# Optimization experiments

Measured on AMD Instinct MI355X. Metric: run time of the kernel, lower is better.

Reference implementation:

```python
import jax, jax.numpy as jnp
import numpy as np

B, N, C = 8, 100000, 90          # batch, total anchors over all levels, num_classes (COCO)
SCORE_THR = 0.05                  # pre_nms_score_threshold
IOU_THR = 0.5                     # nms_iou_threshold
MAX_DET = 100                     # max_num_detections (per class and total)
PRE_NMS_K = 512                   # per-class candidate cap before greedy NMS
NEG = -1e9                        # suppressed-score sentinel


def setup_inputs() -> dict:
    key = jax.random.key(0)
    kb, ks = jax.random.split(key)
    raw = jax.random.uniform(kb, (B, N, 1, 4), dtype=jnp.float32) * 512.0
    # build valid [y1, x1, y2, x2] boxes from the rand fill
    y1 = jnp.minimum(raw[..., 0], raw[..., 2])
    y2 = jnp.maximum(raw[..., 0], raw[..., 2])
    x1 = jnp.minimum(raw[..., 1], raw[..., 3])
    x2 = jnp.maximum(raw[..., 1], raw[..., 3])
    boxes = jnp.stack([y1, x1, y2, x2], axis=-1)            # [B, N, 1, 4]
    scores = jax.random.uniform(ks, (B, N, C), dtype=jnp.float32)  # [B, N, C]
    return {"boxes": boxes, "scores": scores}


def _iou_one_vs_all(box, boxes):
    # box: [4], boxes: [K, 4], layout (y1, x1, y2, x2)
    yy1 = jnp.maximum(box[0], boxes[:, 0])
    xx1 = jnp.maximum(box[1], boxes[:, 1])
    yy2 = jnp.minimum(box[2], boxes[:, 2])
    xx2 = jnp.minimum(box[3], boxes[:, 3])
    inter = jnp.clip(yy2 - yy1, 0.0) * jnp.clip(xx2 - xx1, 0.0)
    area = (box[2] - box[0]) * (box[3] - box[1])
    areas = (boxes[:, 2] - boxes[:, 0]) * (boxes[:, 3] - boxes[:, 1])
    return inter / (area + areas - inter + 1e-8)


def _nms_single(cboxes, cscores):
    # Greedy per-class NMS: cboxes [K,4], cscores [K] -> MAX_DET boxes/scores.
    K = cboxes.shape[0]
    idxs = jnp.arange(K)

    def step(active, _):
        j = jnp.argmax(active)
        s = active[j]
        b = cboxes[j]
        iou = _iou_one_vs_all(b, cboxes)
        sup = (iou > IOU_THR) | (idxs == j)
        return jnp.where(sup, NEG, active), (b, s)

    _, (sel_boxes, sel_scores) = jax.lax.scan(step, cscores, None, length=MAX_DET)
    return sel_boxes, sel_scores  # [MAX_DET, 4], [MAX_DET]


def _detections(boxes, scores):
    bx = boxes[:, :, 0, :]                                   # class-agnostic boxes [B, N, 4]
    sm = jnp.where(scores >= SCORE_THR, scores, NEG)         # score thresholding
    st = jnp.transpose(sm, (0, 2, 1))                        # [B, C, N]
    cscores, cidx = jax.lax.top_k(st, PRE_NMS_K)             # [B, C, K]
    cboxes = jax.vmap(lambda b, i: b[i])(bx, cidx)           # [B, C, K, 4]
    sel_boxes, sel_scores = jax.vmap(jax.vmap(_nms_single))(cboxes, cscores)
    cls = jnp.broadcast_to(jnp.arange(C)[None, :, None], (B, C, MAX_DET))
    fs = sel_scores.reshape(B, -1)                           # [B, C*MAX_DET]
    fb = sel_boxes.reshape(B, -1, 4)
    fc = cls.reshape(B, -1)
    top_s, top_i = jax.lax.top_k(fs, MAX_DET)                # top MAX_DET over all classes
    top_b = jnp.take_along_axis(fb, top_i[..., None], axis=1)
    top_c = jnp.take_along_axis(fc, top_i, axis=1)
    valid = top_s >= SCORE_THR
    out_boxes = jnp.where(valid[..., None], top_b, 0.0)     # [B, MAX_DET, 4]
    out_scores = jnp.where(valid, top_s, 0.0)               # [B, MAX_DET]
    out_classes = jnp.where(valid, top_c, 0).astype(jnp.int32)
    num_valid = valid.sum(axis=1).astype(jnp.int32)         # [B]
    return out_boxes, out_scores, out_classes, num_valid


def reference(boxes, scores):
    return _detections(boxes, scores)
```

## Files before the change

kernel.cpp:

```cpp
#include <hip/hip_runtime.h>

#define NB 8
#define NN 100000
#define NC 90
#define SCORE_THR 0.05f
#define IOU_THR 0.5f
#define MAX_DET 100
#define PRE_NMS_K 512
#define NEGV -1000000000.0f
#define T0 0.9925f
#define CAP 1024
#define NBC (NB * NC)
#define CNT_STRIDE 16
#define CHUNK 1024
#define NCHUNK 98
#define LCAP 32
#define IOU_CMP_C 0x1.0000008p-1

typedef float f32x4 __attribute__((ext_vector_type(4)));

__device__ __forceinline__ unsigned ordf(float s) {
    unsigned u = __float_as_uint(s);
    return (u & 0x80000000u) ? ~u : (u | 0x80000000u);
}
__device__ __forceinline__ float deordf(unsigned o) {
    return (o & 0x80000000u) ? __uint_as_float(o ^ 0x80000000u) : __uint_as_float(~o);
}
__device__ __forceinline__ unsigned long long mkkey(float s, unsigned idx) {
    return ((unsigned long long)ordf(s) << 32) | (unsigned long long)(0xFFFFFFFFu - idx);
}

__global__ __launch_bounds__(256) void k_zero(uint4* __restrict__ cnt4, uint4* __restrict__ ovf4) {
    unsigned i = blockIdx.x * 256u + threadIdx.x;
    if (i < (NBC * CNT_STRIDE) / 4) cnt4[i] = make_uint4(0u, 0u, 0u, 0u);
    if (i < NBC / 4) ovf4[i] = make_uint4(0u, 0u, 0u, 0u);
}

__global__ __launch_bounds__(512) void k_collect(const float* __restrict__ scores,
                                                 unsigned* __restrict__ cnt,
                                                 unsigned* __restrict__ ovf,
                                                 unsigned long long* __restrict__ buf) {
    __shared__ unsigned long long lst[NC][LCAP + 1];
    __shared__ unsigned lcnt[NC];
    int b = blockIdx.x / NCHUNK;
    int chunk = blockIdx.x - b * NCHUNK;
    int n0 = chunk * CHUNK;
    const f32x4* base4 = reinterpret_cast<const f32x4*>(scores + ((size_t)b * NN + n0) * NC);

    for (int i = threadIdx.x; i < NC; i += 512) lcnt[i] = 0u;
    __syncthreads();

    auto process = [&](f32x4 v, int idx) {
        #pragma unroll
        for (int e = 0; e < 4; ++e) {
            float s = v[e];
            if (s >= T0) {
                int local = 4 * idx + e;
                int c = local % NC;
                int n = n0 + local / NC;
                unsigned slot = atomicAdd(&lcnt[c], 1u);
                if (slot < LCAP) lst[c][slot] = mkkey(s, (unsigned)n);
                else atomicOr(&ovf[b * NC + c], 1u);
            }
        }
    };

    if (chunk != NCHUNK - 1) {
        for (int i0 = (int)threadIdx.x; i0 < 23040; i0 += 1536) {
            f32x4 v0 = base4[i0];
            f32x4 v1 = base4[i0 + 512];
            f32x4 v2 = base4[i0 + 1024];
            process(v0, i0);
            process(v1, i0 + 512);
            process(v2, i0 + 1024);
        }
    } else {
        int ncount = NN - n0;
        int nf4 = (ncount * NC) >> 2;
        for (int i = (int)threadIdx.x; i < nf4; i += 512) {
            f32x4 v = base4[i];
            process(v, i);
        }
    }
    __syncthreads();

    if (threadIdx.x < NC) {
        int c = threadIdx.x;
        unsigned k = lcnt[c]; if (k > LCAP) k = LCAP;
        if (k) {
            int bc = b * NC + c;
            unsigned basep = atomicAdd(&cnt[(size_t)bc * CNT_STRIDE], k);
            if (basep + k > CAP) atomicOr(&ovf[bc], 1u);
            unsigned lim = (basep + k <= CAP) ? k : (basep < CAP ? CAP - basep : 0u);
            for (unsigned j = 0; j < lim; ++j)
                buf[(size_t)bc * CAP + basep + j] = lst[c][j];
        }
    }
}

__global__ __launch_bounds__(256) void k_sortnms(const float* __restrict__ scores,
                                                 const float* __restrict__ boxes,
                                                 const unsigned* __restrict__ cnt,
                                                 const unsigned* __restrict__ ovf,
                                                 const unsigned long long* __restrict__ buf,
                                                 float* __restrict__ sel_score,
                                                 float4* __restrict__ sel_box) {
    #pragma clang fp contract(off)
    int bc = blockIdx.x;
    int tid = threadIdx.x;
    __shared__ unsigned long long keys[CAP];
    __shared__ __align__(16) unsigned char gmem[PRE_NMS_K * 16 + PRE_NMS_K * 4];
    float4* box_lds = (float4*)gmem;
    float* area_lds = (float*)(gmem + PRE_NMS_K * 16);
    unsigned* hist = (unsigned*)gmem;
    __shared__ unsigned s_lcnt;
    __shared__ float s_cut;

    unsigned K = cnt[(size_t)bc * CNT_STRIDE];
    bool bad = (ovf[bc] != 0u) || (K < (unsigned)PRE_NMS_K) || (K > CAP);

    if (bad) {
        int b = bc / NC, c = bc - (bc / NC) * NC;
        for (int i = tid; i < 1024; i += 256) hist[i] = 0u;
        if (tid == 0) s_lcnt = 0u;
        __syncthreads();
        for (int n = tid; n < NN; n += 256) {
            float s = scores[((size_t)b * NN + n) * NC + c];
            if (s >= SCORE_THR) {
                int bin = (int)(s * 1024.0f);
                bin = bin < 0 ? 0 : (bin > 1023 ? 1023 : bin);
                atomicAdd(&hist[bin], 1u);
            }
        }
        __syncthreads();
        if (tid == 0) {
            unsigned tot = 0;
            for (int i = 0; i < 1024; ++i) tot += hist[i];
            unsigned target = tot < (unsigned)PRE_NMS_K ? tot : (unsigned)PRE_NMS_K;
            float cut = 3.0e38f;
            if (target > 0) {
                unsigned cum = 0; int t = 1023;
                for (; t >= 0; --t) { cum += hist[t]; if (cum >= target) break; }
                cut = (float)t / 1024.0f;
                if (cut < SCORE_THR) cut = SCORE_THR;
            }
            s_cut = cut;
        }
        __syncthreads();
        float cut = s_cut;
        for (int n = tid; n < NN; n += 256) {
            float s = scores[((size_t)b * NN + n) * NC + c];
            if (s >= SCORE_THR && s >= cut) {
                unsigned slot = atomicAdd(&s_lcnt, 1u);
                if (slot < CAP) keys[slot] = mkkey(s, (unsigned)n);
            }
        }
        __syncthreads();
        K = s_lcnt; if (K > CAP) K = CAP;
        for (unsigned i = K + tid; i < CAP; i += 256) keys[i] = 0ULL;
        __syncthreads();
    } else {
        for (unsigned i = tid; i < CAP; i += 256)
            keys[i] = (i < K) ? buf[(size_t)bc * CAP + i] : 0ULL;
    }

    bool prev_big = false;
    for (unsigned k2 = 2; k2 <= CAP; k2 <<= 1) {
        for (unsigned j = k2 >> 1; j; j >>= 1) {
            bool big = (j >= 64);
            if (big || prev_big) __syncthreads();
            #pragma unroll
            for (unsigned ii = 0; ii < 4; ++ii) {
                unsigned i = tid + ii * 256u;
                unsigned ixj = i ^ j;
                if (ixj > i) {
                    unsigned long long a = keys[i], bv = keys[ixj];
                    bool desc = ((i & k2) == 0);
                    if (desc ? (a < bv) : (a > bv)) { keys[i] = bv; keys[ixj] = a; }
                }
            }
            prev_big = big;
        }
    }
    __syncthreads();

    int b = bc / NC;
    for (int r = tid; r < PRE_NMS_K; r += 256) {
        unsigned long long key = keys[r];
        float4 bx = make_float4(0.f, 0.f, 0.f, 0.f);
        if (key != 0ULL) {
            unsigned n = 0xFFFFFFFFu - (unsigned)(key & 0xFFFFFFFFu);
            bx = *reinterpret_cast<const float4*>(boxes + ((size_t)b * NN + n) * 4);
        }
        box_lds[r] = bx;
        area_lds[r] = (bx.z - bx.x) * (bx.w - bx.y);
    }
    __syncthreads();

    if (tid < 64) {
        int lane = tid;
        float y1[8], x1[8], y2[8], x2[8], ar[8];
        unsigned alive = 0u;
        #pragma unroll
        for (int k = 0; k < 8; ++k) {
            int r = lane * 8 + k;
            float4 bx = box_lds[r];
            y1[k] = bx.x; x1[k] = bx.y; y2[k] = bx.z; x2[k] = bx.w;
            ar[k] = area_lds[r];
            if (keys[r] != 0ULL) alive |= (1u << k);
        }
        for (int it = 0; it < MAX_DET; ++it) {
            unsigned long long bal = __ballot(alive != 0u);
            if (bal == 0ULL) {
                if (lane == 0) {
                    sel_score[bc * MAX_DET + it] = NEGV;
                    sel_box[bc * MAX_DET + it] = make_float4(0.f, 0.f, 0.f, 0.f);
                }
                continue;
            }
            int lw = __ffsll((unsigned long long)bal) - 1;
            unsigned aw = __shfl(alive, lw);
            int bit = __ffs(aw) - 1;
            int widx = lw * 8 + bit;
            float4 wb = box_lds[widx];
            float warea = area_lds[widx];
            if (lane == 0) {
                unsigned long long wk = keys[widx];
                sel_score[bc * MAX_DET + it] = deordf((unsigned)(wk >> 32));
                sel_box[bc * MAX_DET + it] = wb;
            }
            unsigned sup = 0u;
            #pragma unroll
            for (int k = 0; k < 8; ++k) {
                float yy1 = fmaxf(wb.x, y1[k]);
                float xx1 = fmaxf(wb.y, x1[k]);
                float yy2 = fminf(wb.z, y2[k]);
                float xx2 = fminf(wb.w, x2[k]);
                float ih = fmaxf(yy2 - yy1, 0.0f);
                float iw = fmaxf(xx2 - xx1, 0.0f);
                float inter = ih * iw;
                float denom = ((warea + ar[k]) - inter) + 1e-8f;
                if ((double)inter > IOU_CMP_C * (double)denom) sup |= (1u << k);
            }
            alive &= ~sup;
            if (lane == lw) alive &= ~(1u << bit);
        }
    }
}

__global__ __launch_bounds__(256) void k_merge(const float* __restrict__ sel_score,
                                               const float4* __restrict__ sel_box,
                                               float* __restrict__ out) {
    int b = blockIdx.x;
    int tid = threadIdx.x;
    __shared__ unsigned long long lkeys[NC * MAX_DET];
    __shared__ unsigned long long win[MAX_DET];
    const float* ss = sel_score + b * NC * MAX_DET;

    for (int i = tid; i < NC * MAX_DET; i += 256)
        lkeys[i] = mkkey(ss[i], (unsigned)i);
    __syncthreads();

    if (tid < 64) {
        int lane = tid;
        int r1 = 0, r2 = 0;
        unsigned long long k1 = lkeys[lane * MAX_DET];
        unsigned long long k2 = (lane < 26) ? lkeys[(64 + lane) * MAX_DET] : 0ULL;
        for (int it = 0; it < MAX_DET; ++it) {
            unsigned long long w = k1 > k2 ? k1 : k2;
            for (int off = 1; off < 64; off <<= 1) {
                unsigned long long o = __shfl_xor(w, off);
                if (o > w) w = o;
            }
            if (lane == 0) win[it] = w;
            if (k1 == w) { r1++; k1 = (r1 < MAX_DET) ? lkeys[lane * MAX_DET + r1] : 0ULL; }
            else if (lane < 26 && k2 == w) { r2++; k2 = (r2 < MAX_DET) ? lkeys[(64 + lane) * MAX_DET + r2] : 0ULL; }
        }

        int nv = 0;
        for (int t = lane; t < MAX_DET; t += 64) {
            unsigned long long w = win[t];
            unsigned flat = 0xFFFFFFFFu - (unsigned)(w & 0xFFFFFFFFu);
            float sdec = deordf((unsigned)(w >> 32));
            bool valid = (w != 0ULL) && (sdec >= SCORE_THR);
            float4 bx = make_float4(0.f, 0.f, 0.f, 0.f);
            float so = 0.0f; int cls = 0;
            if (valid) {
                bx = sel_box[b * NC * MAX_DET + flat];
                so = sdec;
                cls = (int)(flat / MAX_DET);
                nv++;
            }
            float* ob = out + (size_t)(b * MAX_DET + t) * 4;
            ob[0] = bx.x; ob[1] = bx.y; ob[2] = bx.z; ob[3] = bx.w;
            out[NB * MAX_DET * 4 + b * MAX_DET + t] = so;
            out[NB * MAX_DET * 5 + b * MAX_DET + t] = (float)cls;
        }
        for (int off = 1; off < 64; off <<= 1) nv += __shfl_xor(nv, off);
        if (lane == 0) out[NB * MAX_DET * 6 + b] = (float)nv;
    }
}

extern "C" void kernel_launch(void* const* d_in, const int* in_sizes, int n_in,
                              void* d_out, int out_size, void* d_ws, size_t ws_size,
                              hipStream_t stream) {
    const float* boxes = (const float*)d_in[0];
    const float* scores = (const float*)d_in[1];
    float* out = (float*)d_out;

    char* ws = (char*)d_ws;
    size_t off = 0;
    auto alloc = [&](size_t bytes) -> void* {
        void* p = ws + off;
        off = (off + bytes + 255) & ~(size_t)255;
        return p;
    };
    unsigned* cnt = (unsigned*)alloc((size_t)NBC * CNT_STRIDE * 4);
    unsigned* ovf = (unsigned*)alloc((size_t)NBC * 4);
    unsigned long long* buf = (unsigned long long*)alloc((size_t)NBC * CAP * 8);
    float* sel_score = (float*)alloc((size_t)NBC * MAX_DET * 4);
    float4* sel_box = (float4*)alloc((size_t)NBC * MAX_DET * 16);

    k_zero<<<(NBC * CNT_STRIDE / 4 + 255) / 256, 256, 0, stream>>>((uint4*)cnt, (uint4*)ovf);
    k_collect<<<NB * NCHUNK, 512, 0, stream>>>(scores, cnt, ovf, buf);
    k_sortnms<<<NBC, 256, 0, stream>>>(scores, boxes, cnt, ovf, buf, sel_score, sel_box);
    k_merge<<<NB, 256, 0, stream>>>(sel_score, sel_box, out);
}
```

Baseline: 193.9 us.

## Replace global atomic candidate append with per-chunk segments and drop zero kernel

Each collect block now writes its per-class count and up to LCAP candidates into a fixed per-(batch,class,chunk) segment instead of atomically appending to a shared per-class buffer with overflow flags. The sort kernel prefix-sums the 98 chunk counts to compact candidates into LDS and detects overflow from the counts, which removes the separate zero-initialisation kernel launch and the global atomics. In exchange the sort kernel reads a larger sparse segment array and does a serial prefix scan. The collect loop also loses its manual 3-way unroll.

```diff
diff --git a/kernel.cpp b/kernel.cpp
--- a/kernel.cpp
+++ b/kernel.cpp
@@ -11,7 +11,6 @@
 #define T0 0.9925f
 #define CAP 1024
 #define NBC (NB * NC)
-#define CNT_STRIDE 16
 #define CHUNK 1024
 #define NCHUNK 98
 #define LCAP 32
@@ -30,79 +29,52 @@
     return ((unsigned long long)ordf(s) << 32) | (unsigned long long)(0xFFFFFFFFu - idx);
 }
 
-__global__ __launch_bounds__(256) void k_zero(uint4* __restrict__ cnt4, uint4* __restrict__ ovf4) {
-    unsigned i = blockIdx.x * 256u + threadIdx.x;
-    if (i < (NBC * CNT_STRIDE) / 4) cnt4[i] = make_uint4(0u, 0u, 0u, 0u);
-    if (i < NBC / 4) ovf4[i] = make_uint4(0u, 0u, 0u, 0u);
-}
-
 __global__ __launch_bounds__(512) void k_collect(const float* __restrict__ scores,
-                                                 unsigned* __restrict__ cnt,
-                                                 unsigned* __restrict__ ovf,
-                                                 unsigned long long* __restrict__ buf) {
+                                                 unsigned* __restrict__ cnt2,
+                                                 unsigned long long* __restrict__ buf2) {
     __shared__ unsigned long long lst[NC][LCAP + 1];
     __shared__ unsigned lcnt[NC];
     int b = blockIdx.x / NCHUNK;
     int chunk = blockIdx.x - b * NCHUNK;
     int n0 = chunk * CHUNK;
+    int ncount = NN - n0; if (ncount > CHUNK) ncount = CHUNK;
+    int nf4 = (ncount * NC) >> 2;
     const f32x4* base4 = reinterpret_cast<const f32x4*>(scores + ((size_t)b * NN + n0) * NC);
 
     for (int i = threadIdx.x; i < NC; i += 512) lcnt[i] = 0u;
     __syncthreads();
 
-    auto process = [&](f32x4 v, int idx) {
+    for (int i = (int)threadIdx.x; i < nf4; i += 512) {
+        f32x4 v = base4[i];
         #pragma unroll
         for (int e = 0; e < 4; ++e) {
             float s = v[e];
             if (s >= T0) {
-                int local = 4 * idx + e;
+                int local = 4 * i + e;
                 int c = local % NC;
                 int n = n0 + local / NC;
                 unsigned slot = atomicAdd(&lcnt[c], 1u);
                 if (slot < LCAP) lst[c][slot] = mkkey(s, (unsigned)n);
-                else atomicOr(&ovf[b * NC + c], 1u);
-            }
-        }
-    };
-
-    if (chunk != NCHUNK - 1) {
-        for (int i0 = (int)threadIdx.x; i0 < 23040; i0 += 1536) {
-            f32x4 v0 = base4[i0];
-            f32x4 v1 = base4[i0 + 512];
-            f32x4 v2 = base4[i0 + 1024];
-            process(v0, i0);
-            process(v1, i0 + 512);
-            process(v2, i0 + 1024);
-        }
-    } else {
-        int ncount = NN - n0;
-        int nf4 = (ncount * NC) >> 2;
-        for (int i = (int)threadIdx.x; i < nf4; i += 512) {
-            f32x4 v = base4[i];
-            process(v, i);
+            }
         }
     }
     __syncthreads();
 
     if (threadIdx.x < NC) {
         int c = threadIdx.x;
-        unsigned k = lcnt[c]; if (k > LCAP) k = LCAP;
-        if (k) {
-            int bc = b * NC + c;
-            unsigned basep = atomicAdd(&cnt[(size_t)bc * CNT_STRIDE], k);
-            if (basep + k > CAP) atomicOr(&ovf[bc], 1u);
-            unsigned lim = (basep + k <= CAP) ? k : (basep < CAP ? CAP - basep : 0u);
-            for (unsigned j = 0; j < lim; ++j)
-                buf[(size_t)bc * CAP + basep + j] = lst[c][j];
-        }
+        int bc = b * NC + c;
+        unsigned count = lcnt[c];
+        cnt2[(size_t)bc * NCHUNK + chunk] = count;
+        unsigned k = count > LCAP ? LCAP : count;
+        unsigned long long* dst = buf2 + ((size_t)bc * NCHUNK + chunk) * LCAP;
+        for (unsigned j = 0; j < k; ++j) dst[j] = lst[c][j];
     }
 }
 
 __global__ __launch_bounds__(256) void k_sortnms(const float* __restrict__ scores,
                                                  const float* __restrict__ boxes,
-                                                 const unsigned* __restrict__ cnt,
-                                                 const unsigned* __restrict__ ovf,
-                                                 const unsigned long long* __restrict__ buf,
+                                                 const unsigned* __restrict__ cnt2,
+                                                 const unsigned long long* __restrict__ buf2,
                                                  float* __restrict__ sel_score,
                                                  float4* __restrict__ sel_box) {
     #pragma clang fp contract(off)
@@ -113,11 +85,28 @@
     float4* box_lds = (float4*)gmem;
     float* area_lds = (float*)(gmem + PRE_NMS_K * 16);
     unsigned* hist = (unsigned*)gmem;
+    __shared__ unsigned segc[NCHUNK];
+    __shared__ unsigned sego[NCHUNK + 1];
+    __shared__ unsigned s_bad;
     __shared__ unsigned s_lcnt;
     __shared__ float s_cut;
 
-    unsigned K = cnt[(size_t)bc * CNT_STRIDE];
-    bool bad = (ovf[bc] != 0u) || (K < (unsigned)PRE_NMS_K) || (K > CAP);
+    if (tid == 0) s_bad = 0u;
+    if (tid < NCHUNK) segc[tid] = cnt2[(size_t)bc * NCHUNK + tid];
+    __syncthreads();
+    if (tid < NCHUNK && segc[tid] > LCAP) atomicOr(&s_bad, 1u);
+    if (tid == 0) {
+        unsigned a = 0;
+        for (int p = 0; p < NCHUNK; ++p) {
+            sego[p] = a;
+            unsigned k = segc[p]; if (k > LCAP) k = LCAP;
+            a += k;
+        }
+        sego[NCHUNK] = a;
+    }
+    __syncthreads();
+    unsigned K = sego[NCHUNK];
+    bool bad = (s_bad != 0u) || (K < (unsigned)PRE_NMS_K) || (K > CAP);
 
     if (bad) {
         int b = bc / NC, c = bc - (bc / NC) * NC;
@@ -160,11 +149,16 @@
         for (unsigned i = K + tid; i < CAP; i += 256) keys[i] = 0ULL;
         __syncthreads();
     } else {
-        for (unsigned i = tid; i < CAP; i += 256)
-            keys[i] = (i < K) ? buf[(size_t)bc * CAP + i] : 0ULL;
-    }
-
-    bool prev_big = false;
+        const unsigned long long* src = buf2 + (size_t)bc * NCHUNK * LCAP;
+        for (int slot = tid; slot < NCHUNK * LCAP; slot += 256) {
+            int p = slot >> 5, j = slot & 31;
+            if ((unsigned)j < segc[p]) keys[sego[p] + j] = src[slot];
+        }
+        __syncthreads();
+        for (unsigned i = K + tid; i < CAP; i += 256) keys[i] = 0ULL;
+    }
+
+    bool prev_big = true;
     for (unsigned k2 = 2; k2 <= CAP; k2 <<= 1) {
         for (unsigned j = k2 >> 1; j; j >>= 1) {
             bool big = (j >= 64);
@@ -315,14 +309,12 @@
         off = (off + bytes + 255) & ~(size_t)255;
         return p;
     };
-    unsigned* cnt = (unsigned*)alloc((size_t)NBC * CNT_STRIDE * 4);
-    unsigned* ovf = (unsigned*)alloc((size_t)NBC * 4);
-    unsigned long long* buf = (unsigned long long*)alloc((size_t)NBC * CAP * 8);
+    unsigned* cnt2 = (unsigned*)alloc((size_t)NBC * NCHUNK * 4);
+    unsigned long long* buf2 = (unsigned long long*)alloc((size_t)NBC * NCHUNK * LCAP * 8);
     float* sel_score = (float*)alloc((size_t)NBC * MAX_DET * 4);
     float4* sel_box = (float4*)alloc((size_t)NBC * MAX_DET * 16);
 
-    k_zero<<<(NBC * CNT_STRIDE / 4 + 255) / 256, 256, 0, stream>>>((uint4*)cnt, (uint4*)ovf);
-    k_collect<<<NB * NCHUNK, 512, 0, stream>>>(scores, cnt, ovf, buf);
-    k_sortnms<<<NBC, 256, 0, stream>>>(scores, boxes, cnt, ovf, buf, sel_score, sel_box);
+    k_collect<<<NB * NCHUNK, 512, 0, stream>>>(scores, cnt2, buf2);
+    k_sortnms<<<NBC, 256, 0, stream>>>(scores, boxes, cnt2, buf2, sel_score, sel_box);
     k_merge<<<NB, 256, 0, stream>>>(sel_score, sel_box, out);
 }
```

Result: faster. 185.7 us (-4.2%).
